# Kernel tuning notes

Measured on AMD Instinct MI355X. Metric: run time of the kernel, lower is better.

## Reference

```python
import jax, jax.numpy as jnp
import numpy as np

N = 65536      # batch rows
D = 32         # input_dim (number of per-feature sub-MLPs)
H = 128        # nodes_per_layer_in_sub_fn
# num_hidden_layers_per_feature_fn = 2 -> Linear(1,H),ReLU, Linear(H,H),ReLU, Linear(H,1)


def setup_inputs() -> dict:
    key = jax.random.key(0)
    ks = jax.random.split(key, 7)
    s1 = 1.0            # fan_in=1 kaiming-uniform-ish scale
    sH = 1.0 / np.sqrt(H)
    x = jax.random.normal(ks[0], (N, D), dtype=jnp.float32)
    W1 = jax.random.uniform(ks[1], (D, H), jnp.float32, -s1, s1)      # Linear(1,H) weight per feature
    b1 = jax.random.uniform(ks[2], (D, H), jnp.float32, -s1, s1)
    W2 = jax.random.uniform(ks[3], (D, H, H), jnp.float32, -sH, sH)   # Linear(H,H) per feature
    b2 = jax.random.uniform(ks[4], (D, H), jnp.float32, -sH, sH)
    W3 = jax.random.uniform(ks[5], (D, H), jnp.float32, -sH, sH)      # Linear(H,1) per feature
    b3 = jax.random.uniform(ks[6], (D,), jnp.float32, -sH, sH)
    return {"x": x, "W1": W1, "b1": b1, "W2": W2, "b2": b2, "W3": W3, "b3": b3}


def reference(x, W1, b1, W2, b2, W3, b3):
    # h1[n,d,h] = relu(x[n,d] * W1[d,h] + b1[d,h])
    h1 = jax.nn.relu(x[:, :, None] * W1[None, :, :] + b1[None, :, :])          # [N,D,H]
    # h2: per-feature batched GEMM, Linear(H,H) + ReLU
    h2 = jax.nn.relu(jnp.einsum('ndh,dhk->ndk', h1, W2) + b2[None, :, :])      # [N,D,H]
    # per-feature output Linear(H,1), then sum across features, keepdim
    per_feat = jnp.einsum('ndh,dh->nd', h2, W3) + b3[None, :]                  # [N,D]
    return jnp.sum(per_feat, axis=1, keepdims=True)                            # [N,1]
```

## Files before the change

kernel.cpp:

```cpp
#include <hip/hip_runtime.h>
#include <hip/hip_bf16.h>
#include <stdint.h>


#define D_FEAT 32
#define H_DIM  128
#define SLOTS  24
#define THREADS 256
#define ROWTILES 1024
#define MAXT   43

typedef float    f32x16 __attribute__((ext_vector_type(16)));
typedef short    bf16x8 __attribute__((ext_vector_type(8)));
typedef uint32_t u32;

static __device__ __forceinline__ u32 cvtpk(float lo, float hi) {
    u32 r;
    asm("v_cvt_pk_bf16_f32 %0, %1, %2" : "=v"(r) : "v"(lo), "v"(hi));
    return r;
}
static __device__ __forceinline__ bf16x8 frag4(u32 a, u32 b, u32 c, u32 d) {
    int4 t = make_int4((int)a, (int)b, (int)c, (int)d);
    return __builtin_bit_cast(bf16x8, t);
}
static __device__ __forceinline__ bf16x8 frag1(u32 a) { return frag4(a, 0u, 0u, 0u); }

#define MFMA32(A, B, C) __builtin_amdgcn_mfma_f32_32x32x16_bf16((A), (B), (C), 0, 0, 0)

static __device__ __forceinline__ bf16x8 relu_pack(const f32x16& v, int s) {
    u32 c0 = cvtpk(fmaxf(v[8*s+0], 0.f), fmaxf(v[8*s+1], 0.f));
    u32 c1 = cvtpk(fmaxf(v[8*s+2], 0.f), fmaxf(v[8*s+3], 0.f));
    u32 c2 = cvtpk(fmaxf(v[8*s+4], 0.f), fmaxf(v[8*s+5], 0.f));
    u32 c3 = cvtpk(fmaxf(v[8*s+6], 0.f), fmaxf(v[8*s+7], 0.f));
    return frag4(c0, c1, c2, c3);
}

__global__ __launch_bounds__(THREADS, 3) void kan_main(
    const float* __restrict__ x,
    const float* __restrict__ W1,
    const float* __restrict__ b1,
    const float* __restrict__ W2,
    const float* __restrict__ b2,
    const float* __restrict__ W3,
    const float* __restrict__ b3,
    float* __restrict__ out)
{
    __shared__ float xall[MAXT * 64];
    __shared__ float W3s[H_DIM];

    const int tid   = threadIdx.x;
    const int d     = blockIdx.x / SLOTS;
    const int bslot = blockIdx.x % SLOTS;
    const int w     = tid >> 6;
    const int wm    = w >> 1;
    const int wn    = w & 1;
    const int l     = tid & 63;
    const int l31   = l & 31;
    const int g     = l >> 5;

    const int ntile = (ROWTILES - 1 - bslot) / SLOTS + 1;

    for (int idx = tid; idx < ntile * 64; idx += THREADS) {
        int tl = idx >> 6;
        xall[idx] = x[(size_t)((bslot + SLOTS * tl) * 64 + (idx & 63)) * D_FEAT + d];
    }
    if (tid < H_DIM) W3s[tid] = W3[d * H_DIM + tid];

    float b3s = 0.f;
#pragma unroll
    for (int k = 0; k < D_FEAT; ++k) b3s += b3[k];

    const int mo0 = 2 * wm, mo1 = 2 * wm + 1;
    u32 w1b1[4], b2w[2];
#pragma unroll
    for (int mt = 0; mt < 4; ++mt) {
        int m = 32 * mt + l31;
        u32 v = cvtpk(W1[d * H_DIM + m], b1[d * H_DIM + m]);
        w1b1[mt] = g ? 0u : v;
    }
    b2w[0] = g ? 0u : cvtpk(b2[d * H_DIM + 32 * mo0 + l31], 0.f);
    b2w[1] = g ? 0u : cvtpk(b2[d * H_DIM + 32 * mo1 + l31], 0.f);
    const bf16x8 onesB = frag1(g ? 0u : 0x00003F80u);

    bf16x8 w2f[2][8];
    {
        const float* W2d = W2 + (size_t)d * H_DIM * H_DIM;
#pragma unroll
        for (int j = 0; j < 2; ++j) {
            int mm = 32 * (mo0 + j) + l31;
#pragma unroll
            for (int ks = 0; ks < 8; ++ks) {
                u32 dw[4];
#pragma unroll
                for (int p = 0; p < 4; ++p) {
                    int e0 = 2 * p, e1 = 2 * p + 1;
                    int k0 = 16 * ks + 4 * g + (e0 & 3) + 8 * (e0 >> 2);
                    int k1 = 16 * ks + 4 * g + (e1 & 3) + 8 * (e1 >> 2);
                    dw[p] = cvtpk(W2d[(size_t)k0 * H_DIM + mm],
                                  W2d[(size_t)k1 * H_DIM + mm]);
                }
                w2f[j][ks] = frag4(dw[0], dw[1], dw[2], dw[3]);
            }
        }
    }
    __syncthreads();

    const f32x16 zc = {};
    const bool addb3 = (d == 0) && (wm == 0);

    for (int it = 0; it < ntile; ++it) {
        const int rbase = (bslot + SLOTS * it) * 64 + 32 * wn;
        float xv = xall[it * 64 + 32 * wn + l31];
        bf16x8 Bx = frag1(g ? 0u : cvtpk(xv, 1.0f));

        f32x16 a0 = MFMA32(frag1(b2w[0]), onesB, zc);
        f32x16 a1 = MFMA32(frag1(b2w[1]), onesB, zc);

#pragma unroll
        for (int mt = 0; mt < 4; ++mt) {
            f32x16 d1 = MFMA32(frag1(w1b1[mt]), Bx, zc);
            bf16x8 bl = relu_pack(d1, 0);
            bf16x8 bh = relu_pack(d1, 1);
            a0 = MFMA32(w2f[0][2 * mt + 0], bl, a0);
            a1 = MFMA32(w2f[1][2 * mt + 0], bl, a1);
            a0 = MFMA32(w2f[0][2 * mt + 1], bh, a0);
            a1 = MFMA32(w2f[1][2 * mt + 1], bh, a1);
        }

        float rs = 0.f;
#pragma unroll
        for (int q = 0; q < 4; ++q) {
            const float4 w3a = *reinterpret_cast<const float4*>(&W3s[32 * mo0 + 4 * g + 8 * q]);
            const float4 w3b = *reinterpret_cast<const float4*>(&W3s[32 * mo1 + 4 * g + 8 * q]);
            rs += fmaxf(a0[4 * q + 0], 0.f) * w3a.x;
            rs += fmaxf(a0[4 * q + 1], 0.f) * w3a.y;
            rs += fmaxf(a0[4 * q + 2], 0.f) * w3a.z;
            rs += fmaxf(a0[4 * q + 3], 0.f) * w3a.w;
            rs += fmaxf(a1[4 * q + 0], 0.f) * w3b.x;
            rs += fmaxf(a1[4 * q + 1], 0.f) * w3b.y;
            rs += fmaxf(a1[4 * q + 2], 0.f) * w3b.z;
            rs += fmaxf(a1[4 * q + 3], 0.f) * w3b.w;
        }
        rs += __shfl_xor(rs, 32, 64);
        if (addb3) rs += b3s;
        if (!g) atomicAdd(&out[rbase + l31], rs);
    }
}

extern "C" void kernel_launch(void* const* d_in, const int* in_sizes, int n_in,
                              void* d_out, int out_size, void* d_ws, size_t ws_size,
                              hipStream_t stream) {
    const float* x  = (const float*)d_in[0];
    const float* W1 = (const float*)d_in[1];
    const float* b1 = (const float*)d_in[2];
    const float* W2 = (const float*)d_in[3];
    const float* b2 = (const float*)d_in[4];
    const float* W3 = (const float*)d_in[5];
    const float* b3 = (const float*)d_in[6];
    float* out = (float*)d_out;
    const int N = in_sizes[0] / D_FEAT;

    hipMemsetAsync(out, 0, (size_t)N * sizeof(float), stream);
    kan_main<<<D_FEAT * SLOTS, THREADS, 0, stream>>>(x, W1, b1, W2, b2, W3, b3, out);
}
```

Before: 158.0 us.

## Process two row tiles per iteration and rebalance grid to 16 slots

The main loop now handles two 64-row tiles at once with independent MFMA accumulator chains, giving the matrix units more independent work to hide dependent-MFMA latency. The grid shrinks from 24 to 16 slots per feature, so every block does a fixed 64 tiles and the x staging loop can be fully unrolled. The epilogue uses fma with split partial sums for shorter dependency chains. The cost is higher register pressure, with occupancy lowered to 2 blocks per SM, and fewer blocks overall, which risks leaving CUs underused.

```diff
diff --git a/kernel.cpp b/kernel.cpp
--- a/kernel.cpp
+++ b/kernel.cpp
@@ -5,10 +5,9 @@
 
 #define D_FEAT 32
 #define H_DIM  128
-#define SLOTS  24
+#define SLOTS  16
 #define THREADS 256
-#define ROWTILES 1024
-#define MAXT   43
+#define NTILE  64
 
 typedef float    f32x16 __attribute__((ext_vector_type(16)));
 typedef short    bf16x8 __attribute__((ext_vector_type(8)));
@@ -35,7 +34,29 @@
     return frag4(c0, c1, c2, c3);
 }
 
-__global__ __launch_bounds__(THREADS, 3) void kan_main(
+static __device__ __forceinline__ float epi(const f32x16& a0, const f32x16& a1,
+                                            const float* __restrict__ W3s,
+                                            int mo0, int mo1, int g) {
+    float p[4];
+#pragma unroll
+    for (int q = 0; q < 4; ++q) {
+        const float4 wa = *reinterpret_cast<const float4*>(&W3s[32 * mo0 + 4 * g + 8 * q]);
+        const float4 wb = *reinterpret_cast<const float4*>(&W3s[32 * mo1 + 4 * g + 8 * q]);
+        float t;
+        t = fmaxf(a0[4*q+0], 0.f) * wa.x;
+        t = fmaf(fmaxf(a0[4*q+1], 0.f), wa.y, t);
+        t = fmaf(fmaxf(a0[4*q+2], 0.f), wa.z, t);
+        t = fmaf(fmaxf(a0[4*q+3], 0.f), wa.w, t);
+        t = fmaf(fmaxf(a1[4*q+0], 0.f), wb.x, t);
+        t = fmaf(fmaxf(a1[4*q+1], 0.f), wb.y, t);
+        t = fmaf(fmaxf(a1[4*q+2], 0.f), wb.z, t);
+        t = fmaf(fmaxf(a1[4*q+3], 0.f), wb.w, t);
+        p[q] = t;
+    }
+    return (p[0] + p[1]) + (p[2] + p[3]);
+}
+
+__global__ __launch_bounds__(THREADS, 2) void kan_main(
     const float* __restrict__ x,
     const float* __restrict__ W1,
     const float* __restrict__ b1,
@@ -45,7 +66,7 @@
     const float* __restrict__ b3,
     float* __restrict__ out)
 {
-    __shared__ float xall[MAXT * 64];
+    __shared__ float xall[NTILE * 64];
     __shared__ float W3s[H_DIM];
 
     const int tid   = threadIdx.x;
@@ -58,10 +79,10 @@
     const int l31   = l & 31;
     const int g     = l >> 5;
 
-    const int ntile = (ROWTILES - 1 - bslot) / SLOTS + 1;
-
-    for (int idx = tid; idx < ntile * 64; idx += THREADS) {
-        int tl = idx >> 6;
+#pragma unroll
+    for (int i = 0; i < (NTILE * 64) / THREADS; ++i) {
+        int idx = tid + THREADS * i;
+        int tl  = idx >> 6;
         xall[idx] = x[(size_t)((bslot + SLOTS * tl) * 64 + (idx & 63)) * D_FEAT + d];
     }
     if (tid < H_DIM) W3s[tid] = W3[d * H_DIM + tid];
@@ -108,42 +129,44 @@
     const f32x16 zc = {};
     const bool addb3 = (d == 0) && (wm == 0);
 
-    for (int it = 0; it < ntile; ++it) {
-        const int rbase = (bslot + SLOTS * it) * 64 + 32 * wn;
-        float xv = xall[it * 64 + 32 * wn + l31];
-        bf16x8 Bx = frag1(g ? 0u : cvtpk(xv, 1.0f));
+    for (int ip = 0; ip < NTILE; ip += 2) {
+        const int rb0 = (bslot + SLOTS * (ip + 0)) * 64 + 32 * wn;
+        const int rb1 = (bslot + SLOTS * (ip + 1)) * 64 + 32 * wn;
+        float xv0 = xall[(ip + 0) * 64 + 32 * wn + l31];
+        float xv1 = xall[(ip + 1) * 64 + 32 * wn + l31];
+        bf16x8 Bx0 = frag1(g ? 0u : cvtpk(xv0, 1.0f));
+        bf16x8 Bx1 = frag1(g ? 0u : cvtpk(xv1, 1.0f));
 
-        f32x16 a0 = MFMA32(frag1(b2w[0]), onesB, zc);
-        f32x16 a1 = MFMA32(frag1(b2w[1]), onesB, zc);
+        f32x16 a00 = MFMA32(frag1(b2w[0]), onesB, zc);
+        f32x16 a01 = MFMA32(frag1(b2w[1]), onesB, zc);
+        f32x16 a10 = MFMA32(frag1(b2w[0]), onesB, zc);
+        f32x16 a11 = MFMA32(frag1(b2w[1]), onesB, zc);
 
 #pragma unroll
         for (int mt = 0; mt < 4; ++mt) {
-            f32x16 d1 = MFMA32(frag1(w1b1[mt]), Bx, zc);
-            bf16x8 bl = relu_pack(d1, 0);
-            bf16x8 bh = relu_pack(d1, 1);
-            a0 = MFMA32(w2f[0][2 * mt + 0], bl, a0);
-            a1 = MFMA32(w2f[1][2 * mt + 0], bl, a1);
-            a0 = MFMA32(w2f[0][2 * mt + 1], bh, a0);
-            a1 = MFMA32(w2f[1][2 * mt + 1], bh, a1);
+            f32x16 d10 = MFMA32(frag1(w1b1[mt]), Bx0, zc);
+            f32x16 d11 = MFMA32(frag1(w1b1[mt]), Bx1, zc);
+            bf16x8 bl0 = relu_pack(d10, 0), bh0 = relu_pack(d10, 1);
+            bf16x8 bl1 = relu_pack(d11, 0), bh1 = relu_pack(d11, 1);
+            a00 = MFMA32(w2f[0][2 * mt + 0], bl0, a00);
+            a10 = MFMA32(w2f[0][2 * mt + 0], bl1, a10);
+            a01 = MFMA32(w2f[1][2 * mt + 0], bl0, a01);
+            a11 = MFMA32(w2f[1][2 * mt + 0], bl1, a11);
+            a00 = MFMA32(w2f[0][2 * mt + 1], bh0, a00);
+            a10 = MFMA32(w2f[0][2 * mt + 1], bh1, a10);
+            a01 = MFMA32(w2f[1][2 * mt + 1], bh0, a01);
+            a11 = MFMA32(w2f[1][2 * mt + 1], bh1, a11);
         }
 
-        float rs = 0.f;
-#pragma unroll
-        for (int q = 0; q < 4; ++q) {
-            const float4 w3a = *reinterpret_cast<const float4*>(&W3s[32 * mo0 + 4 * g + 8 * q]);
-            const float4 w3b = *reinterpret_cast<const float4*>(&W3s[32 * mo1 + 4 * g + 8 * q]);
-            rs += fmaxf(a0[4 * q + 0], 0.f) * w3a.x;
-            rs += fmaxf(a0[4 * q + 1], 0.f) * w3a.y;
-            rs += fmaxf(a0[4 * q + 2], 0.f) * w3a.z;
-            rs += fmaxf(a0[4 * q + 3], 0.f) * w3a.w;
-            rs += fmaxf(a1[4 * q + 0], 0.f) * w3b.x;
-            rs += fmaxf(a1[4 * q + 1], 0.f) * w3b.y;
-            rs += fmaxf(a1[4 * q + 2], 0.f) * w3b.z;
-            rs += fmaxf(a1[4 * q + 3], 0.f) * w3b.w;
+        float rs0 = epi(a00, a01, W3s, mo0, mo1, g);
+        float rs1 = epi(a10, a11, W3s, mo0, mo1, g);
+        rs0 += __shfl_xor(rs0, 32, 64);
+        rs1 += __shfl_xor(rs1, 32, 64);
+        if (addb3) { rs0 += b3s; rs1 += b3s; }
+        if (!g) {
+            atomicAdd(&out[rb0 + l31], rs0);
+            atomicAdd(&out[rb1 + l31], rs1);
         }
-        rs += __shfl_xor(rs, 32, 64);
-        if (addb3) rs += b3s;
-        if (!g) atomicAdd(&out[rbase + l31], rs);
     }
 }
 
```

Measured after the change: 160.4 us. No clear change (+1.6%).
